# Kernel tuning notes

Measured on AMD Instinct MI355X. Metric: run time of the kernel, lower is better.

## Reference

```python
import jax, jax.numpy as jnp
import numpy as np

EPS = 1e-6

def _log_g(x):
    # log of continuous g(x) = where(x>=0, x+0.5, sigmoid(x)) from minGRU paper
    return jnp.where(x >= 0, jnp.log(jax.nn.relu(x) + 0.5), -jax.nn.softplus(-x))

def setup_inputs() -> dict:
    key = jax.random.key(0)
    ks = jax.random.split(key, 4)
    B, S, D, E = 4, 2048, 1024, 8
    scale = D ** -0.5
    return {
        "inputs": jax.random.normal(ks[0], (B, S, D), dtype=jnp.float32),
        "norm_weight": jnp.ones((D,), jnp.float32),
        "router_w": jax.random.normal(ks[1], (E, D), jnp.float32) * scale,
        "router_b": jnp.zeros((E,), jnp.float32),
        "w_hg": jax.random.normal(ks[2], (E, 2 * D, D), jnp.float32) * scale,
        "w_out": jax.random.normal(ks[3], (E, D, D), jnp.float32) * scale,
    }

def reference(inputs, norm_weight, router_w, router_b, w_hg, w_out):
    D = inputs.shape[-1]
    # --- RMSNorm ---
    x = inputs * jax.lax.rsqrt(jnp.mean(inputs * inputs, axis=-1, keepdims=True) + EPS) * norm_weight
    # --- SMEAR: per-sample soft merge of expert weights via mean-pooled routing ---
    probs = jax.nn.softmax(jnp.mean(x, axis=1) @ router_w.T + router_b, axis=-1)  # [B,E]
    W_hg = jnp.einsum('be,ekd->bkd', probs, w_hg)    # [B,2D,D] merged to_hidden_and_gate
    W_out = jnp.einsum('be,eod->bod', probs, w_out)  # [B,D,D]  merged to_out
    # --- minGRU with merged weights (log-space parallel scan, no initial state) ---
    hg = jnp.einsum('bsd,bkd->bsk', x, W_hg)         # [B,S,2D]
    hidden, gate = hg[..., :D], hg[..., D:]
    log_coeffs = -jax.nn.softplus(gate)                      # log(1 - z_t)
    log_values = -jax.nn.softplus(-gate) + _log_g(hidden)    # log z_t + log g(h~_t)
    a_star = jnp.cumsum(log_coeffs, axis=1)
    log_h = a_star + jax.lax.cumlogsumexp(log_values - a_star, axis=1)
    h = jnp.exp(log_h)                               # [B,S,D] recurrent states
    new_state = h[:, -1:]                            # [B,1,D]
    out = jnp.einsum('bsk,bok->bso', h, W_out)       # proj_out
    aux_loss = jnp.zeros((), inputs.dtype)
    return (out + inputs, new_state, aux_loss)
```

## Files before the change

### kernel.cpp

```cpp
#include <hip/hip_runtime.h>
#include <hip/hip_bf16.h>

#define B_  4
#define S_  2048
#define D_  1024
#define E_  8
#define K2_ 2048

#define CHUNKS 64
#define CLEN   32

typedef __attribute__((ext_vector_type(8))) short short8;
typedef __attribute__((ext_vector_type(4))) float floatx4;

__device__ __forceinline__ void gld16(const void* g, const void* l) {
    __builtin_amdgcn_global_load_lds(
        (const __attribute__((address_space(1))) unsigned int*)g,
        (__attribute__((address_space(3))) unsigned int*)l, 16, 0, 0);
}

__global__ void rmsnorm_k(const float* __restrict__ in, const float* __restrict__ nw,
                          __hip_bfloat16* __restrict__ x) {
    int b = blockIdx.y, s = blockIdx.x, t = threadIdx.x;
    const float* row = in + ((size_t)b * S_ + s) * D_;
    float v[4]; float ss = 0.0f;
#pragma unroll
    for (int i = 0; i < 4; i++) { v[i] = row[t + 256 * i]; ss += v[i] * v[i]; }
#pragma unroll
    for (int o = 32; o > 0; o >>= 1) ss += __shfl_down(ss, o, 64);
    __shared__ float ls[4];
    if ((t & 63) == 0) ls[t >> 6] = ss;
    __syncthreads();
    float tot = ls[0] + ls[1] + ls[2] + ls[3];
    float rs = rsqrtf(tot * (1.0f / (float)D_) + 1e-6f);
    __hip_bfloat16* xr = x + ((size_t)b * S_ + s) * D_;
#pragma unroll
    for (int i = 0; i < 4; i++)
        xr[t + 256 * i] = __float2bfloat16(v[i] * rs * nw[t + 256 * i]);
}

__global__ void xsum_k(const __hip_bfloat16* __restrict__ x, float* __restrict__ xs) {
    int d = blockIdx.x * 256 + threadIdx.x;
    int b = blockIdx.y;
    int s0 = blockIdx.z * 128;
    const __hip_bfloat16* p = x + ((size_t)b * S_ + s0) * D_ + d;
    float acc = 0.0f;
#pragma unroll 4
    for (int s = 0; s < 128; s++) { acc += __bfloat162float(*p); p += D_; }
    atomicAdd(&xs[b * D_ + d], acc);
}

__global__ void router_k(const float* __restrict__ xs, const float* __restrict__ rw,
                         const float* __restrict__ rb, float* __restrict__ probs,
                         float* __restrict__ aux) {
    int t = threadIdx.x;
    if (t == 255) *aux = 0.0f;
    int pair = t >> 3, sub = t & 7;
    int b = pair >> 3, e = pair & 7;
    float acc = 0.0f;
    for (int d = sub; d < D_; d += 8) acc += xs[b * D_ + d] * rw[e * D_ + d];
#pragma unroll
    for (int o = 4; o > 0; o >>= 1) acc += __shfl_down(acc, o, 8);
    __shared__ float lg[32];
    if (sub == 0) lg[pair] = acc * (1.0f / (float)S_) + rb[e];
    __syncthreads();
    if (t < 4) {
        float m = -1e30f;
        for (int e2 = 0; e2 < 8; e2++) m = fmaxf(m, lg[t * 8 + e2]);
        float ssum = 0.0f; float ex[8];
        for (int e2 = 0; e2 < 8; e2++) { ex[e2] = expf(lg[t * 8 + e2] - m); ssum += ex[e2]; }
        for (int e2 = 0; e2 < 8; e2++) probs[t * 8 + e2] = ex[e2] / ssum;
    }
}

__global__ void mix_k(const float* __restrict__ probs, const float* __restrict__ whg_e,
                      const float* __restrict__ wout_e, __hip_bfloat16* __restrict__ Whg,
                      __hip_bfloat16* __restrict__ Wout) {
    __shared__ float P[32];
    int t = threadIdx.x;
    if (t < 32) P[t] = probs[t];
    __syncthreads();
    size_t i = (size_t)blockIdx.x * 256 + t;
    const size_t T1 = (size_t)K2_ * D_;
    const size_t T2 = (size_t)D_ * D_;
    if (i < T1) {
        float a0 = 0, a1 = 0, a2 = 0, a3 = 0;
#pragma unroll
        for (int e = 0; e < 8; e++) {
            float w = whg_e[(size_t)e * T1 + i];
            a0 += P[0 * 8 + e] * w; a1 += P[1 * 8 + e] * w;
            a2 += P[2 * 8 + e] * w; a3 += P[3 * 8 + e] * w;
        }
        Whg[0 * T1 + i] = __float2bfloat16(a0); Whg[1 * T1 + i] = __float2bfloat16(a1);
        Whg[2 * T1 + i] = __float2bfloat16(a2); Whg[3 * T1 + i] = __float2bfloat16(a3);
    } else {
        size_t j = i - T1;
        float a0 = 0, a1 = 0, a2 = 0, a3 = 0;
#pragma unroll
        for (int e = 0; e < 8; e++) {
            float w = wout_e[(size_t)e * T2 + j];
            a0 += P[0 * 8 + e] * w; a1 += P[1 * 8 + e] * w;
            a2 += P[2 * 8 + e] * w; a3 += P[3 * 8 + e] * w;
        }
        Wout[0 * T2 + j] = __float2bfloat16(a0); Wout[1 * T2 + j] = __float2bfloat16(a1);
        Wout[2 * T2 + j] = __float2bfloat16(a2); Wout[3 * T2 + j] = __float2bfloat16(a3);
    }
}

__global__ __launch_bounds__(256) void gemm_hg_cv(
    const __hip_bfloat16* __restrict__ A, const __hip_bfloat16* __restrict__ Bm,
    float* __restrict__ cv) {
    const int K = D_;
    int bz = blockIdx.z;
    A  += (size_t)bz * S_ * D_;
    Bm += (size_t)bz * K2_ * D_;
    float2* CV = (float2*)cv + (size_t)bz * S_ * D_;
    int m0 = blockIdx.y * 128, n0 = blockIdx.x * 64;
    __shared__ __hip_bfloat16 lA[128][64];
    __shared__ __hip_bfloat16 lBh[64][64];
    __shared__ __hip_bfloat16 lBg[64][64];
    int t = threadIdx.x;
    int w = t >> 6, lane = t & 63;
    int lm = lane & 15, quad = lane >> 4;
    int wr = w >> 1, wc = w & 1;
    floatx4 acch[4][2] = {};
    floatx4 accg[4][2] = {};
    int srow = lane >> 3;
    int swzb = ((lane & 7) ^ srow) * 16;
    const __hip_bfloat16* Bh = Bm;
    const __hip_bfloat16* Bg = Bm + (size_t)D_ * K;

    for (int k0 = 0; k0 < K; k0 += 64) {
#pragma unroll
        for (int it = 0; it < 4; it++) {
            int r0 = (w * 4 + it) * 8;
            gld16((const char*)(A + (size_t)(m0 + r0 + srow) * K + k0) + swzb,
                  &lA[r0][0]);
        }
#pragma unroll
        for (int it = 0; it < 2; it++) {
            int r0 = (w * 2 + it) * 8;
            gld16((const char*)(Bh + (size_t)(n0 + r0 + srow) * K + k0) + swzb,
                  &lBh[r0][0]);
            gld16((const char*)(Bg + (size_t)(n0 + r0 + srow) * K + k0) + swzb,
                  &lBg[r0][0]);
        }
        __syncthreads();
#pragma unroll
        for (int kk = 0; kk < 64; kk += 32) {
            short8 af[4], bh[2], bg[2];
#pragma unroll
            for (int i = 0; i < 4; i++) {
                int p = (((kk >> 3) + quad) ^ (lm & 7)) * 8;
                af[i] = *(const short8*)(&lA[wr * 64 + i * 16 + lm][p]);
            }
#pragma unroll
            for (int j = 0; j < 2; j++) {
                int p = (((kk >> 3) + quad) ^ (lm & 7)) * 8;
                bh[j] = *(const short8*)(&lBh[wc * 32 + j * 16 + lm][p]);
                bg[j] = *(const short8*)(&lBg[wc * 32 + j * 16 + lm][p]);
            }
#pragma unroll
            for (int i = 0; i < 4; i++)
#pragma unroll
                for (int j = 0; j < 2; j++) {
                    acch[i][j] = __builtin_amdgcn_mfma_f32_16x16x32_bf16(
                        af[i], bh[j], acch[i][j], 0, 0, 0);
                    accg[i][j] = __builtin_amdgcn_mfma_f32_16x16x32_bf16(
                        af[i], bg[j], accg[i][j], 0, 0, 0);
                }
        }
        __syncthreads();
    }
#pragma unroll
    for (int i = 0; i < 4; i++) {
#pragma unroll
        for (int j = 0; j < 2; j++) {
#pragma unroll
            for (int r = 0; r < 4; r++) {
                int m = m0 + wr * 64 + i * 16 + quad * 4 + r;
                int n = n0 + wc * 32 + j * 16 + lm;
                float hid = acch[i][j][r];
                float g   = accg[i][j][r];
                float c  = 1.0f / (1.0f + expf(g));
                float sg = 1.0f / (1.0f + expf(-g));
                float gfn = (hid >= 0.0f) ? (hid + 0.5f)
                                          : (1.0f / (1.0f + expf(-hid)));
                CV[(size_t)m * D_ + n] = make_float2(c, sg * gfn);
            }
        }
    }
}

#define TM 128
#define TN 128
#define TBK 64
__global__ __launch_bounds__(256) void gemm_bf16_bt(
    const __hip_bfloat16* __restrict__ A, const __hip_bfloat16* __restrict__ Bm,
    float* __restrict__ C, const float* __restrict__ R,
    int M, int N, int K, size_t sa, size_t sb, size_t sc, size_t sr) {
    int bz = blockIdx.z;
    A += (size_t)bz * sa; Bm += (size_t)bz * sb; C += (size_t)bz * sc;
    if (R) R += (size_t)bz * sr;
    int m0 = blockIdx.y * TM, n0 = blockIdx.x * TN;
    __shared__ __hip_bfloat16 lA[TM][TBK];
    __shared__ __hip_bfloat16 lB[TN][TBK];
    int t = threadIdx.x;
    int w = t >> 6, lane = t & 63;
    int lm = lane & 15, quad = lane >> 4;
    int wr = w >> 1, wc = w & 1;
    floatx4 acc[4][4] = {};
    int srow = lane >> 3;
    int swzb = ((lane & 7) ^ srow) * 16;

    for (int k0 = 0; k0 < K; k0 += TBK) {
#pragma unroll
        for (int it = 0; it < 4; it++) {
            int r0 = (w * 4 + it) * 8;
            gld16((const char*)(A + (size_t)(m0 + r0 + srow) * K + k0) + swzb,
                  &lA[r0][0]);
            gld16((const char*)(Bm + (size_t)(n0 + r0 + srow) * K + k0) + swzb,
                  &lB[r0][0]);
        }
        __syncthreads();
#pragma unroll
        for (int kk = 0; kk < TBK; kk += 32) {
            short8 af[4], bf[4];
#pragma unroll
            for (int i = 0; i < 4; i++) {
                int p = (((kk >> 3) + quad) ^ (lm & 7)) * 8;
                af[i] = *(const short8*)(&lA[wr * 64 + i * 16 + lm][p]);
            }
#pragma unroll
            for (int j = 0; j < 4; j++) {
                int p = (((kk >> 3) + quad) ^ (lm & 7)) * 8;
                bf[j] = *(const short8*)(&lB[wc * 64 + j * 16 + lm][p]);
            }
#pragma unroll
            for (int i = 0; i < 4; i++)
#pragma unroll
                for (int j = 0; j < 4; j++)
                    acc[i][j] = __builtin_amdgcn_mfma_f32_16x16x32_bf16(
                        af[i], bf[j], acc[i][j], 0, 0, 0);
        }
        __syncthreads();
    }
#pragma unroll
    for (int i = 0; i < 4; i++) {
#pragma unroll
        for (int j = 0; j < 4; j++) {
#pragma unroll
            for (int r = 0; r < 4; r++) {
                int m = m0 + wr * 64 + i * 16 + quad * 4 + r;
                int n = n0 + wc * 64 + j * 16 + lm;
                float v = acc[i][j][r];
                if (R) v += R[(size_t)m * N + n];
                C[(size_t)m * N + n] = v;
            }
        }
    }
}

__global__ void scanA_k(const float* __restrict__ cv, float* __restrict__ Cc,
                        float* __restrict__ Vc) {
    int b = blockIdx.z, c = blockIdx.y;
    int d2 = blockIdx.x * 256 + threadIdx.x;
    const float4* p = (const float4*)cv + (size_t)(b * S_ + c * CLEN) * (D_ / 2) + d2;
    float P0 = 1.0f, V0 = 0.0f, P1 = 1.0f, V1 = 0.0f;
#pragma unroll 4
    for (int s = 0; s < CLEN; s++) {
        float4 e = p[(size_t)s * (D_ / 2)];
        P0 *= e.x; V0 = e.x * V0 + e.y;
        P1 *= e.z; V1 = e.z * V1 + e.w;
    }
    size_t idx = ((size_t)(b * CHUNKS + c)) * D_ + 2 * d2;
    Cc[idx] = P0; Vc[idx] = V0; Cc[idx + 1] = P1; Vc[idx + 1] = V1;
}

__global__ void scanB_k(const float* __restrict__ Cc, const float* __restrict__ Vc,
                        float* __restrict__ Hi) {
    int b = blockIdx.y;
    int d = blockIdx.x * 256 + threadIdx.x;
    float h = 0.0f;
    for (int c = 0; c < CHUNKS; c++) {
        size_t idx = ((size_t)(b * CHUNKS + c)) * D_ + d;
        Hi[idx] = h;
        h = Cc[idx] * h + Vc[idx];
    }
}

__global__ void scanC_k(const float* __restrict__ cv, const float* __restrict__ Hi,
                        __hip_bfloat162* __restrict__ hout, float* __restrict__ ns) {
    int b = blockIdx.z, c = blockIdx.y;
    int d2 = blockIdx.x * 256 + threadIdx.x;
    const float4* p = (const float4*)cv + (size_t)(b * S_ + c * CLEN) * (D_ / 2) + d2;
    size_t hidx = ((size_t)(b * CHUNKS + c)) * D_ + 2 * d2;
    float h0 = Hi[hidx], h1 = Hi[hidx + 1];
#pragma unroll 4
    for (int s = 0; s < CLEN; s++) {
        float4 e = p[(size_t)s * (D_ / 2)];
        h0 = e.x * h0 + e.y;
        h1 = e.z * h1 + e.w;
        __hip_bfloat162 hh;
        hh.x = __float2bfloat16(h0); hh.y = __float2bfloat16(h1);
        hout[(size_t)(b * S_ + c * CLEN + s) * (D_ / 2) + d2] = hh;
    }
    if (c == CHUNKS - 1) { ns[b * D_ + 2 * d2] = h0; ns[b * D_ + 2 * d2 + 1] = h1; }
}

extern "C" void kernel_launch(void* const* d_in, const int* in_sizes, int n_in,
                              void* d_out_v, int out_size, void* d_ws, size_t ws_size,
                              hipStream_t stream) {
    const float* inputs = (const float*)d_in[0];
    const float* nw     = (const float*)d_in[1];
    const float* rw     = (const float*)d_in[2];
    const float* rb     = (const float*)d_in[3];
    const float* whg_e  = (const float*)d_in[4];
    const float* wout_e = (const float*)d_in[5];
    float* out = (float*)d_out_v;

    float* ws = (float*)d_ws;
    float*          cv      = ws;
    __hip_bfloat16* x_bf    = (__hip_bfloat16*)(ws + 16777216);
    __hip_bfloat16* h_bf    = (__hip_bfloat16*)(ws + 20971520);
    __hip_bfloat16* Whg_bf  = (__hip_bfloat16*)(ws + 25165824);
    __hip_bfloat16* Wout_bf = (__hip_bfloat16*)(ws + 29360128);
    float* xsum  = ws + 31457280;
    float* probs = ws + 31461376;
    float* Cc    = ws + 31461408;
    float* Vc    = ws + 31723552;
    float* Hi    = ws + 31985696;

    hipMemsetAsync(xsum, 0, (size_t)B_ * D_ * sizeof(float), stream);

    rmsnorm_k<<<dim3(S_, B_), 256, 0, stream>>>(inputs, nw, x_bf);
    xsum_k<<<dim3(D_ / 256, B_, 16), 256, 0, stream>>>(x_bf, xsum);
    router_k<<<1, 256, 0, stream>>>(xsum, rw, rb, probs,
                                    out + (size_t)B_ * S_ * D_ + (size_t)B_ * D_);
    mix_k<<<12288, 256, 0, stream>>>(probs, whg_e, wout_e, Whg_bf, Wout_bf);

    gemm_hg_cv<<<dim3(D_ / 64, S_ / 128, B_), 256, 0, stream>>>(x_bf, Whg_bf, cv);

    scanA_k<<<dim3(D_ / 512, CHUNKS, B_), 256, 0, stream>>>(cv, Cc, Vc);
    scanB_k<<<dim3(D_ / 256, B_), 256, 0, stream>>>(Cc, Vc, Hi);
    scanC_k<<<dim3(D_ / 512, CHUNKS, B_), 256, 0, stream>>>(
        cv, Hi, (__hip_bfloat162*)h_bf, out + (size_t)B_ * S_ * D_);

    gemm_bf16_bt<<<dim3(D_ / TN, S_ / TM, B_), 256, 0, stream>>>(
        h_bf, Wout_bf, out, inputs, S_, D_, D_,
        (size_t)S_ * D_, (size_t)D_ * D_, (size_t)S_ * D_, (size_t)S_ * D_);
}
```

Before: 345.9 us.

## Store scan coefficients as fp16, vectorize norm/mix, fold chunk-prefix scan into scanC

The gated GRU intermediate (decay coefficient and value pair) is now written as a half2 instead of a float2, which halves the traffic between the hidden/gate GEMM and the two scan passes. The separate inter-chunk scan kernel is removed; each scanC block recomputes its prefix state serially from the per-chunk summaries. RMSNorm and the expert weight mixing are vectorized to float4 loads with packed bf16 stores through a manual round-to-nearest conversion. The costs are fp16 precision loss in the coefficients, redundant prefix work that grows with the chunk index, and fewer blocks in the scan kernels.

```diff
diff --git a/kernel.cpp b/kernel.cpp
--- a/kernel.cpp
+++ b/kernel.cpp
@@ -1,5 +1,6 @@
 #include <hip/hip_runtime.h>
 #include <hip/hip_bf16.h>
+#include <hip/hip_fp16.h>
 
 #define B_  4
 #define S_  2048
@@ -19,13 +20,18 @@
         (__attribute__((address_space(3))) unsigned int*)l, 16, 0, 0);
 }
 
+__device__ __forceinline__ unsigned short f2bf(float f) {
+    unsigned int u = __float_as_uint(f);
+    u += 0x7fffu + ((u >> 16) & 1u);
+    return (unsigned short)(u >> 16);
+}
+
 __global__ void rmsnorm_k(const float* __restrict__ in, const float* __restrict__ nw,
                           __hip_bfloat16* __restrict__ x) {
     int b = blockIdx.y, s = blockIdx.x, t = threadIdx.x;
-    const float* row = in + ((size_t)b * S_ + s) * D_;
-    float v[4]; float ss = 0.0f;
-#pragma unroll
-    for (int i = 0; i < 4; i++) { v[i] = row[t + 256 * i]; ss += v[i] * v[i]; }
+    const float4* row = (const float4*)(in + ((size_t)b * S_ + s) * D_);
+    float4 v = row[t];
+    float ss = v.x * v.x + v.y * v.y + v.z * v.z + v.w * v.w;
 #pragma unroll
     for (int o = 32; o > 0; o >>= 1) ss += __shfl_down(ss, o, 64);
     __shared__ float ls[4];
@@ -33,10 +39,11 @@
     __syncthreads();
     float tot = ls[0] + ls[1] + ls[2] + ls[3];
     float rs = rsqrtf(tot * (1.0f / (float)D_) + 1e-6f);
-    __hip_bfloat16* xr = x + ((size_t)b * S_ + s) * D_;
-#pragma unroll
-    for (int i = 0; i < 4; i++)
-        xr[t + 256 * i] = __float2bfloat16(v[i] * rs * nw[t + 256 * i]);
+    float4 w = ((const float4*)nw)[t];
+    ushort4 o;
+    o.x = f2bf(v.x * rs * w.x); o.y = f2bf(v.y * rs * w.y);
+    o.z = f2bf(v.z * rs * w.z); o.w = f2bf(v.w * rs * w.w);
+    ((ushort4*)(x + ((size_t)b * S_ + s) * D_))[t] = o;
 }
 
 __global__ void xsum_k(const __hip_bfloat16* __restrict__ x, float* __restrict__ xs) {
@@ -80,41 +87,64 @@
     int t = threadIdx.x;
     if (t < 32) P[t] = probs[t];
     __syncthreads();
-    size_t i = (size_t)blockIdx.x * 256 + t;
-    const size_t T1 = (size_t)K2_ * D_;
-    const size_t T2 = (size_t)D_ * D_;
-    if (i < T1) {
-        float a0 = 0, a1 = 0, a2 = 0, a3 = 0;
+    size_t i4 = (size_t)blockIdx.x * 256 + t;
+    const size_t T1q = (size_t)K2_ * D_ / 4;
+    const size_t T2q = (size_t)D_ * D_ / 4;
+    float4 a0 = {0,0,0,0}, a1 = {0,0,0,0}, a2 = {0,0,0,0}, a3 = {0,0,0,0};
+    if (i4 < T1q) {
+        const float4* src = (const float4*)whg_e;
 #pragma unroll
         for (int e = 0; e < 8; e++) {
-            float w = whg_e[(size_t)e * T1 + i];
-            a0 += P[0 * 8 + e] * w; a1 += P[1 * 8 + e] * w;
-            a2 += P[2 * 8 + e] * w; a3 += P[3 * 8 + e] * w;
-        }
-        Whg[0 * T1 + i] = __float2bfloat16(a0); Whg[1 * T1 + i] = __float2bfloat16(a1);
-        Whg[2 * T1 + i] = __float2bfloat16(a2); Whg[3 * T1 + i] = __float2bfloat16(a3);
+            float4 wv = src[(size_t)e * T1q + i4];
+            float p0 = P[e], p1 = P[8 + e], p2 = P[16 + e], p3 = P[24 + e];
+            a0.x += p0 * wv.x; a0.y += p0 * wv.y; a0.z += p0 * wv.z; a0.w += p0 * wv.w;
+            a1.x += p1 * wv.x; a1.y += p1 * wv.y; a1.z += p1 * wv.z; a1.w += p1 * wv.w;
+            a2.x += p2 * wv.x; a2.y += p2 * wv.y; a2.z += p2 * wv.z; a2.w += p2 * wv.w;
+            a3.x += p3 * wv.x; a3.y += p3 * wv.y; a3.z += p3 * wv.z; a3.w += p3 * wv.w;
+        }
+        ushort4* dst = (ushort4*)Whg;
+        ushort4 o;
+        o.x = f2bf(a0.x); o.y = f2bf(a0.y); o.z = f2bf(a0.z); o.w = f2bf(a0.w);
+        dst[0 * T1q + i4] = o;
+        o.x = f2bf(a1.x); o.y = f2bf(a1.y); o.z = f2bf(a1.z); o.w = f2bf(a1.w);
+        dst[1 * T1q + i4] = o;
+        o.x = f2bf(a2.x); o.y = f2bf(a2.y); o.z = f2bf(a2.z); o.w = f2bf(a2.w);
+        dst[2 * T1q + i4] = o;
+        o.x = f2bf(a3.x); o.y = f2bf(a3.y); o.z = f2bf(a3.z); o.w = f2bf(a3.w);
+        dst[3 * T1q + i4] = o;
     } else {
-        size_t j = i - T1;
-        float a0 = 0, a1 = 0, a2 = 0, a3 = 0;
+        size_t j4 = i4 - T1q;
+        const float4* src = (const float4*)wout_e;
 #pragma unroll
         for (int e = 0; e < 8; e++) {
-            float w = wout_e[(size_t)e * T2 + j];
-            a0 += P[0 * 8 + e] * w; a1 += P[1 * 8 + e] * w;
-            a2 += P[2 * 8 + e] * w; a3 += P[3 * 8 + e] * w;
-        }
-        Wout[0 * T2 + j] = __float2bfloat16(a0); Wout[1 * T2 + j] = __float2bfloat16(a1);
-        Wout[2 * T2 + j] = __float2bfloat16(a2); Wout[3 * T2 + j] = __float2bfloat16(a3);
+            float4 wv = src[(size_t)e * T2q + j4];
+            float p0 = P[e], p1 = P[8 + e], p2 = P[16 + e], p3 = P[24 + e];
+            a0.x += p0 * wv.x; a0.y += p0 * wv.y; a0.z += p0 * wv.z; a0.w += p0 * wv.w;
+            a1.x += p1 * wv.x; a1.y += p1 * wv.y; a1.z += p1 * wv.z; a1.w += p1 * wv.w;
+            a2.x += p2 * wv.x; a2.y += p2 * wv.y; a2.z += p2 * wv.z; a2.w += p2 * wv.w;
+            a3.x += p3 * wv.x; a3.y += p3 * wv.y; a3.z += p3 * wv.z; a3.w += p3 * wv.w;
+        }
+        ushort4* dst = (ushort4*)Wout;
+        ushort4 o;
+        o.x = f2bf(a0.x); o.y = f2bf(a0.y); o.z = f2bf(a0.z); o.w = f2bf(a0.w);
+        dst[0 * T2q + j4] = o;
+        o.x = f2bf(a1.x); o.y = f2bf(a1.y); o.z = f2bf(a1.z); o.w = f2bf(a1.w);
+        dst[1 * T2q + j4] = o;
+        o.x = f2bf(a2.x); o.y = f2bf(a2.y); o.z = f2bf(a2.z); o.w = f2bf(a2.w);
+        dst[2 * T2q + j4] = o;
+        o.x = f2bf(a3.x); o.y = f2bf(a3.y); o.z = f2bf(a3.z); o.w = f2bf(a3.w);
+        dst[3 * T2q + j4] = o;
     }
 }
 
 __global__ __launch_bounds__(256) void gemm_hg_cv(
     const __hip_bfloat16* __restrict__ A, const __hip_bfloat16* __restrict__ Bm,
-    float* __restrict__ cv) {
+    __half2* __restrict__ cv) {
     const int K = D_;
     int bz = blockIdx.z;
     A  += (size_t)bz * S_ * D_;
     Bm += (size_t)bz * K2_ * D_;
-    float2* CV = (float2*)cv + (size_t)bz * S_ * D_;
+    __half2* CV = cv + (size_t)bz * S_ * D_;
     int m0 = blockIdx.y * 128, n0 = blockIdx.x * 64;
     __shared__ __hip_bfloat16 lA[128][64];
     __shared__ __hip_bfloat16 lBh[64][64];
@@ -127,6 +157,7 @@
     floatx4 accg[4][2] = {};
     int srow = lane >> 3;
     int swzb = ((lane & 7) ^ srow) * 16;
+
     const __hip_bfloat16* Bh = Bm;
     const __hip_bfloat16* Bg = Bm + (size_t)D_ * K;
 
@@ -149,14 +180,12 @@
 #pragma unroll
         for (int kk = 0; kk < 64; kk += 32) {
             short8 af[4], bh[2], bg[2];
-#pragma unroll
-            for (int i = 0; i < 4; i++) {
-                int p = (((kk >> 3) + quad) ^ (lm & 7)) * 8;
+            int p = (((kk >> 3) + quad) ^ (lm & 7)) * 8;
+#pragma unroll
+            for (int i = 0; i < 4; i++)
                 af[i] = *(const short8*)(&lA[wr * 64 + i * 16 + lm][p]);
-            }
 #pragma unroll
             for (int j = 0; j < 2; j++) {
-                int p = (((kk >> 3) + quad) ^ (lm & 7)) * 8;
                 bh[j] = *(const short8*)(&lBh[wc * 32 + j * 16 + lm][p]);
                 bg[j] = *(const short8*)(&lBg[wc * 32 + j * 16 + lm][p]);
             }
@@ -186,7 +215,7 @@
                 float sg = 1.0f / (1.0f + expf(-g));
                 float gfn = (hid >= 0.0f) ? (hid + 0.5f)
                                           : (1.0f / (1.0f + expf(-hid)));
-                CV[(size_t)m * D_ + n] = make_float2(c, sg * gfn);
+                CV[(size_t)m * D_ + n] = __floats2half2_rn(c, sg * gfn);
             }
         }
     }
@@ -226,16 +255,13 @@
 #pragma unroll
         for (int kk = 0; kk < TBK; kk += 32) {
             short8 af[4], bf[4];
-#pragma unroll
-            for (int i = 0; i < 4; i++) {
-                int p = (((kk >> 3) + quad) ^ (lm & 7)) * 8;
+            int p = (((kk >> 3) + quad) ^ (lm & 7)) * 8;
+#pragma unroll
+            for (int i = 0; i < 4; i++)
                 af[i] = *(const short8*)(&lA[wr * 64 + i * 16 + lm][p]);
-            }
-#pragma unroll
-            for (int j = 0; j < 4; j++) {
-                int p = (((kk >> 3) + quad) ^ (lm & 7)) * 8;
+#pragma unroll
+            for (int j = 0; j < 4; j++)
                 bf[j] = *(const short8*)(&lB[wc * 64 + j * 16 + lm][p]);
-            }
 #pragma unroll
             for (int i = 0; i < 4; i++)
 #pragma unroll
@@ -261,51 +287,59 @@
     }
 }
 
-__global__ void scanA_k(const float* __restrict__ cv, float* __restrict__ Cc,
+__global__ void scanA_k(const __half2* __restrict__ cv, float* __restrict__ Cc,
                         float* __restrict__ Vc) {
-    int b = blockIdx.z, c = blockIdx.y;
-    int d2 = blockIdx.x * 256 + threadIdx.x;
-    const float4* p = (const float4*)cv + (size_t)(b * S_ + c * CLEN) * (D_ / 2) + d2;
-    float P0 = 1.0f, V0 = 0.0f, P1 = 1.0f, V1 = 0.0f;
+    int c = blockIdx.x, b = blockIdx.y, t = threadIdx.x;
+    const float4* p = (const float4*)(cv + (size_t)(b * S_ + c * CLEN) * D_) + t;
+    float P0 = 1, P1 = 1, P2 = 1, P3 = 1;
+    float V0 = 0, V1 = 0, V2 = 0, V3 = 0;
 #pragma unroll 4
     for (int s = 0; s < CLEN; s++) {
-        float4 e = p[(size_t)s * (D_ / 2)];
-        P0 *= e.x; V0 = e.x * V0 + e.y;
-        P1 *= e.z; V1 = e.z * V1 + e.w;
-    }
-    size_t idx = ((size_t)(b * CHUNKS + c)) * D_ + 2 * d2;
-    Cc[idx] = P0; Vc[idx] = V0; Cc[idx + 1] = P1; Vc[idx + 1] = V1;
-}
-
-__global__ void scanB_k(const float* __restrict__ Cc, const float* __restrict__ Vc,
-                        float* __restrict__ Hi) {
-    int b = blockIdx.y;
-    int d = blockIdx.x * 256 + threadIdx.x;
-    float h = 0.0f;
-    for (int c = 0; c < CHUNKS; c++) {
-        size_t idx = ((size_t)(b * CHUNKS + c)) * D_ + d;
-        Hi[idx] = h;
-        h = Cc[idx] * h + Vc[idx];
-    }
-}
-
-__global__ void scanC_k(const float* __restrict__ cv, const float* __restrict__ Hi,
-                        __hip_bfloat162* __restrict__ hout, float* __restrict__ ns) {
-    int b = blockIdx.z, c = blockIdx.y;
-    int d2 = blockIdx.x * 256 + threadIdx.x;
-    const float4* p = (const float4*)cv + (size_t)(b * S_ + c * CLEN) * (D_ / 2) + d2;
-    size_t hidx = ((size_t)(b * CHUNKS + c)) * D_ + 2 * d2;
-    float h0 = Hi[hidx], h1 = Hi[hidx + 1];
+        float4 raw = p[(size_t)s * (D_ / 4)];
+        const __half2* e = (const __half2*)&raw;
+        float c0 = __low2float(e[0]), v0 = __high2float(e[0]);
+        float c1 = __low2float(e[1]), v1 = __high2float(e[1]);
+        float c2 = __low2float(e[2]), v2 = __high2float(e[2]);
+        float c3 = __low2float(e[3]), v3 = __high2float(e[3]);
+        P0 *= c0; V0 = fmaf(c0, V0, v0);
+        P1 *= c1; V1 = fmaf(c1, V1, v1);
+        P2 *= c2; V2 = fmaf(c2, V2, v2);
+        P3 *= c3; V3 = fmaf(c3, V3, v3);
+    }
+    size_t q = ((size_t)(b * CHUNKS + c)) * (D_ / 4) + t;
+    ((float4*)Cc)[q] = make_float4(P0, P1, P2, P3);
+    ((float4*)Vc)[q] = make_float4(V0, V1, V2, V3);
+}
+
+__global__ void scanC_k(const __half2* __restrict__ cv, const float* __restrict__ Cc,
+                        const float* __restrict__ Vc,
+                        __hip_bfloat16* __restrict__ hout, float* __restrict__ ns) {
+    int c = blockIdx.x, b = blockIdx.y, t = threadIdx.x;
+    float h0 = 0, h1 = 0, h2 = 0, h3 = 0;
+#pragma unroll 4
+    for (int cc = 0; cc < c; cc++) {
+        size_t q = ((size_t)(b * CHUNKS + cc)) * (D_ / 4) + t;
+        float4 C4 = ((const float4*)Cc)[q];
+        float4 V4 = ((const float4*)Vc)[q];
+        h0 = fmaf(C4.x, h0, V4.x); h1 = fmaf(C4.y, h1, V4.y);
+        h2 = fmaf(C4.z, h2, V4.z); h3 = fmaf(C4.w, h3, V4.w);
+    }
+    const float4* p = (const float4*)(cv + (size_t)(b * S_ + c * CLEN) * D_) + t;
+    ushort4* hq = (ushort4*)(hout + (size_t)(b * S_ + c * CLEN) * D_) + t;
 #pragma unroll 4
     for (int s = 0; s < CLEN; s++) {
-        float4 e = p[(size_t)s * (D_ / 2)];
-        h0 = e.x * h0 + e.y;
-        h1 = e.z * h1 + e.w;
-        __hip_bfloat162 hh;
-        hh.x = __float2bfloat16(h0); hh.y = __float2bfloat16(h1);
-        hout[(size_t)(b * S_ + c * CLEN + s) * (D_ / 2) + d2] = hh;
-    }
-    if (c == CHUNKS - 1) { ns[b * D_ + 2 * d2] = h0; ns[b * D_ + 2 * d2 + 1] = h1; }
+        float4 raw = p[(size_t)s * (D_ / 4)];
+        const __half2* e = (const __half2*)&raw;
+        h0 = fmaf(__low2float(e[0]), h0, __high2float(e[0]));
+        h1 = fmaf(__low2float(e[1]), h1, __high2float(e[1]));
+        h2 = fmaf(__low2float(e[2]), h2, __high2float(e[2]));
+        h3 = fmaf(__low2float(e[3]), h3, __high2float(e[3]));
+        ushort4 o;
+        o.x = f2bf(h0); o.y = f2bf(h1); o.z = f2bf(h2); o.w = f2bf(h3);
+        hq[(size_t)s * (D_ / 4)] = o;
+    }
+    if (c == CHUNKS - 1)
+        ((float4*)(ns + (size_t)b * D_))[t] = make_float4(h0, h1, h2, h3);
 }
 
 extern "C" void kernel_launch(void* const* d_in, const int* in_sizes, int n_in,
@@ -320,16 +354,15 @@
     float* out = (float*)d_out_v;
 
     float* ws = (float*)d_ws;
-    float*          cv      = ws;
-    __hip_bfloat16* x_bf    = (__hip_bfloat16*)(ws + 16777216);
-    __hip_bfloat16* h_bf    = (__hip_bfloat16*)(ws + 20971520);
-    __hip_bfloat16* Whg_bf  = (__hip_bfloat16*)(ws + 25165824);
-    __hip_bfloat16* Wout_bf = (__hip_bfloat16*)(ws + 29360128);
-    float* xsum  = ws + 31457280;
-    float* probs = ws + 31461376;
-    float* Cc    = ws + 31461408;
-    float* Vc    = ws + 31723552;
-    float* Hi    = ws + 31985696;
+    __half2*        cv      = (__half2*)ws;
+    __hip_bfloat16* x_bf    = (__hip_bfloat16*)(ws + 8388608);
+    __hip_bfloat16* h_bf    = (__hip_bfloat16*)(ws + 12582912);
+    __hip_bfloat16* Whg_bf  = (__hip_bfloat16*)(ws + 16777216);
+    __hip_bfloat16* Wout_bf = (__hip_bfloat16*)(ws + 20971520);
+    float* xsum  = ws + 23068672;
+    float* probs = ws + 23072768;
+    float* Cc    = ws + 23072800;
+    float* Vc    = ws + 23334944;
 
     hipMemsetAsync(xsum, 0, (size_t)B_ * D_ * sizeof(float), stream);
 
@@ -337,14 +370,13 @@
     xsum_k<<<dim3(D_ / 256, B_, 16), 256, 0, stream>>>(x_bf, xsum);
     router_k<<<1, 256, 0, stream>>>(xsum, rw, rb, probs,
                                     out + (size_t)B_ * S_ * D_ + (size_t)B_ * D_);
-    mix_k<<<12288, 256, 0, stream>>>(probs, whg_e, wout_e, Whg_bf, Wout_bf);
+    mix_k<<<3072, 256, 0, stream>>>(probs, whg_e, wout_e, Whg_bf, Wout_bf);
 
     gemm_hg_cv<<<dim3(D_ / 64, S_ / 128, B_), 256, 0, stream>>>(x_bf, Whg_bf, cv);
 
-    scanA_k<<<dim3(D_ / 512, CHUNKS, B_), 256, 0, stream>>>(cv, Cc, Vc);
-    scanB_k<<<dim3(D_ / 256, B_), 256, 0, stream>>>(Cc, Vc, Hi);
-    scanC_k<<<dim3(D_ / 512, CHUNKS, B_), 256, 0, stream>>>(
-        cv, Hi, (__hip_bfloat162*)h_bf, out + (size_t)B_ * S_ * D_);
+    scanA_k<<<dim3(CHUNKS, B_), 256, 0, stream>>>(cv, Cc, Vc);
+    scanC_k<<<dim3(CHUNKS, B_), 256, 0, stream>>>(
+        cv, Cc, Vc, h_bf, out + (size_t)B_ * S_ * D_);
 
     gemm_bf16_bt<<<dim3(D_ / TN, S_ / TM, B_), 256, 0, stream>>>(
         h_bf, Wout_bf, out, inputs, S_, D_, D_,
```

Result: faster. 330.2 us (-4.5%).
